# Kernel optimization log

Measured on AMD Instinct MI355X. Metric: run time of the kernel, lower is better.

Reference implementation:

```python
import jax, jax.numpy as jnp
import numpy as np
from jax import lax

EPS = 1e-06
NUM_FEATURES = 2048


def _welford(xr, mean0, var0):
    """Sequential Welford running mean/var, exactly matching the torch loop.

    xr: [N, F] rows processed one at a time.
    Update for the n-th observation (n starts at 1):
      if n > 1: var = (n-2)/(n-1)*var + (obs-mean)^2/n
      mean += (obs-mean)/n
    """
    n_rows = xr.shape[0]

    def step(carry, inp):
        mean, var = carry
        obs, n = inp
        nf = n.astype(xr.dtype)
        d = obs - mean
        # safe denominator so the unselected branch at n==1 is finite
        var_new = jnp.where(n > 1, (nf - 2.0) / jnp.maximum(nf - 1.0, 1.0) * var + d * d / nf, var)
        mean_new = mean + d / nf
        return (mean_new, var_new), None

    ns = jnp.arange(1, n_rows + 1, dtype=jnp.int32)
    (mean, var), _ = lax.scan(step, (mean0, var0), (xr, ns))
    return mean, var


def setup_inputs() -> dict:
    key = jax.random.key(0)
    x = jax.random.normal(key, (8192, NUM_FEATURES), dtype=jnp.float32)
    running_mean = jnp.zeros((NUM_FEATURES,), dtype=jnp.float32)
    running_var = jnp.ones((NUM_FEATURES,), dtype=jnp.float32)
    return {"x": x, "running_mean": running_mean, "running_var": running_var}


def reference(x, running_mean, running_var):
    xr = x.reshape(-1, NUM_FEATURES)
    mean, var = _welford(xr, running_mean, running_var)
    # normalize with the FINAL running stats (loop completes before return)
    return (x - mean) / jnp.sqrt(var + EPS)
```

## Files before the change

kernel.cpp:

```cpp
#include <hip/hip_runtime.h>

constexpr int F = 2048;
constexpr int NROWS = 8192;
constexpr float EPS = 1e-6f;
constexpr int STRIDE4 = F / 4;

__global__ __launch_bounds__(256) void reduce_kernel(const float* __restrict__ x,
                                                     float* __restrict__ acc) {
    __shared__ float4 lS[3 * 64];
    __shared__ float4 lQ[3 * 64];

    const int lc = threadIdx.x & 63;
    const int sg = threadIdx.x >> 6;
    const int c4 = blockIdx.x * 64 + lc;
    const int row0 = blockIdx.y * 64 + sg * 16;
    const float4* __restrict__ xv = reinterpret_cast<const float4*>(x);

    float4 s = make_float4(0.f, 0.f, 0.f, 0.f);
    float4 q = make_float4(0.f, 0.f, 0.f, 0.f);

    size_t base = (size_t)row0 * STRIDE4 + (size_t)c4;
#pragma unroll
    for (int r = 0; r < 16; ++r) {
        float4 v = xv[base + (size_t)r * STRIDE4];
        s.x += v.x;  s.y += v.y;  s.z += v.z;  s.w += v.w;
        q.x += v.x * v.x;  q.y += v.y * v.y;  q.z += v.z * v.z;  q.w += v.w * v.w;
    }

    if (sg != 0) {
        lS[(sg - 1) * 64 + lc] = s;
        lQ[(sg - 1) * 64 + lc] = q;
    }
    __syncthreads();

    if (sg == 0) {
#pragma unroll
        for (int k = 0; k < 3; ++k) {
            float4 t = lS[k * 64 + lc];
            float4 u = lQ[k * 64 + lc];
            s.x += t.x;  s.y += t.y;  s.z += t.z;  s.w += t.w;
            q.x += u.x;  q.y += u.y;  q.z += u.z;  q.w += u.w;
        }
        float* __restrict__ sum   = acc;
        float* __restrict__ sumsq = acc + F;
        const int c = c4 * 4;
        atomicAdd(&sum[c + 0], s.x);
        atomicAdd(&sum[c + 1], s.y);
        atomicAdd(&sum[c + 2], s.z);
        atomicAdd(&sum[c + 3], s.w);
        atomicAdd(&sumsq[c + 0], q.x);
        atomicAdd(&sumsq[c + 1], q.y);
        atomicAdd(&sumsq[c + 2], q.z);
        atomicAdd(&sumsq[c + 3], q.w);
    }
}

__global__ void finalize_kernel(const float* __restrict__ acc, float* __restrict__ stats) {
    const int c = blockIdx.x * blockDim.x + threadIdx.x;
    if (c < F) {
        const float s1 = acc[c];
        const float s2 = acc[c + F];
        const float invN = 1.0f / (float)NROWS;
        const float mean = s1 * invN;
        float var = (s2 - s1 * mean) * (1.0f / (float)(NROWS - 1));
        var = fmaxf(var, 0.0f);
        const float r = rsqrtf(var + EPS);
        stats[c]     = r;
        stats[c + F] = -mean * r;
    }
}

constexpr int TOTAL4 = NROWS * STRIDE4;
constexpr int HALF4  = TOTAL4 / 2;

__global__ __launch_bounds__(256) void normalize_kernel(const float* __restrict__ x,
                                                        const float* __restrict__ stats,
                                                        float* __restrict__ out) {
    const size_t i = (size_t)blockIdx.x * blockDim.x + threadIdx.x;
    const float4* __restrict__ xv = reinterpret_cast<const float4*>(x);
    float4* __restrict__ ov       = reinterpret_cast<float4*>(out);
    const float4* __restrict__ rv = reinterpret_cast<const float4*>(stats);
    const float4* __restrict__ bv = reinterpret_cast<const float4*>(stats + F);

#pragma unroll
    for (int h = 0; h < 2; ++h) {
        const size_t idx = i + (size_t)h * HALF4;
        const int c4 = (int)(idx & (STRIDE4 - 1));
        float4 v = xv[idx];
        float4 r = rv[c4];
        float4 b = bv[c4];
        float4 o;
        o.x = fmaf(v.x, r.x, b.x);
        o.y = fmaf(v.y, r.y, b.y);
        o.z = fmaf(v.z, r.z, b.z);
        o.w = fmaf(v.w, r.w, b.w);
        ov[idx] = o;
    }
}

extern "C" void kernel_launch(void* const* d_in, const int* in_sizes, int n_in,
                              void* d_out, int out_size, void* d_ws, size_t ws_size,
                              hipStream_t stream) {
    const float* x = (const float*)d_in[0];
    float* out   = (float*)d_out;
    float* acc   = (float*)d_ws;
    float* stats = acc + 2 * F;

    hipMemsetAsync(d_ws, 0, 2 * F * sizeof(float), stream);

    reduce_kernel<<<dim3(8, NROWS / 64), 256, 0, stream>>>(x, acc);
    finalize_kernel<<<F / 256, 256, 0, stream>>>(acc, stats);
    normalize_kernel<<<HALF4 / 256, 256, 0, stream>>>(x, stats, out);
}
```

Baseline: 131.2 us.

## Fuse finalize into normalize kernel and use nontemporal output stores

Removes the separate finalize kernel: each normalize thread now derives scale and bias for its four columns directly from the accumulated sums, and processes 16 rows with the same tiling as the reduce kernel. The output is written with nontemporal stores so it does not pollute cache, and the sum-of-squares accumulation uses fmaf. This saves one kernel launch and a round trip through the stats buffer, at the cost of redundant per-thread stat computation and a different access pattern in the normalize pass.

```diff
diff --git a/kernel.cpp b/kernel.cpp
--- a/kernel.cpp
+++ b/kernel.cpp
@@ -4,6 +4,8 @@
 constexpr int NROWS = 8192;
 constexpr float EPS = 1e-6f;
 constexpr int STRIDE4 = F / 4;
+
+typedef float nfloat4 __attribute__((ext_vector_type(4)));
 
 __global__ __launch_bounds__(256) void reduce_kernel(const float* __restrict__ x,
                                                      float* __restrict__ acc) {
@@ -24,7 +26,10 @@
     for (int r = 0; r < 16; ++r) {
         float4 v = xv[base + (size_t)r * STRIDE4];
         s.x += v.x;  s.y += v.y;  s.z += v.z;  s.w += v.w;
-        q.x += v.x * v.x;  q.y += v.y * v.y;  q.z += v.z * v.z;  q.w += v.w * v.w;
+        q.x = fmaf(v.x, v.x, q.x);
+        q.y = fmaf(v.y, v.y, q.y);
+        q.z = fmaf(v.z, v.z, q.z);
+        q.w = fmaf(v.w, v.w, q.w);
     }
 
     if (sg != 0) {
@@ -55,46 +60,53 @@
     }
 }
 
-__global__ void finalize_kernel(const float* __restrict__ acc, float* __restrict__ stats) {
-    const int c = blockIdx.x * blockDim.x + threadIdx.x;
-    if (c < F) {
-        const float s1 = acc[c];
-        const float s2 = acc[c + F];
-        const float invN = 1.0f / (float)NROWS;
-        const float mean = s1 * invN;
-        float var = (s2 - s1 * mean) * (1.0f / (float)(NROWS - 1));
-        var = fmaxf(var, 0.0f);
-        const float r = rsqrtf(var + EPS);
-        stats[c]     = r;
-        stats[c + F] = -mean * r;
+__global__ __launch_bounds__(256) void norm_kernel(const float* __restrict__ x,
+                                                   const float* __restrict__ acc,
+                                                   float* __restrict__ out) {
+    const int lc = threadIdx.x & 63;
+    const int sg = threadIdx.x >> 6;
+    const int c4 = blockIdx.x * 64 + lc;
+    const int row0 = blockIdx.y * 64 + sg * 16;
+    const float4* __restrict__ xv = reinterpret_cast<const float4*>(x);
+    nfloat4* __restrict__ ov      = reinterpret_cast<nfloat4*>(out);
+
+    const float4 S1 = reinterpret_cast<const float4*>(acc)[c4];
+    const float4 S2 = reinterpret_cast<const float4*>(acc + F)[c4];
+
+    const float invN  = 1.0f / (float)NROWS;
+    const float invN1 = 1.0f / (float)(NROWS - 1);
+
+    float4 r4, b4;
+    {
+        const float mx = S1.x * invN;
+        const float my = S1.y * invN;
+        const float mz = S1.z * invN;
+        const float mw = S1.w * invN;
+        const float vx = fmaxf((S2.x - S1.x * mx) * invN1, 0.0f);
+        const float vy = fmaxf((S2.y - S1.y * my) * invN1, 0.0f);
+        const float vz = fmaxf((S2.z - S1.z * mz) * invN1, 0.0f);
+        const float vw = fmaxf((S2.w - S1.w * mw) * invN1, 0.0f);
+        r4.x = rsqrtf(vx + EPS);
+        r4.y = rsqrtf(vy + EPS);
+        r4.z = rsqrtf(vz + EPS);
+        r4.w = rsqrtf(vw + EPS);
+        b4.x = -mx * r4.x;
+        b4.y = -my * r4.y;
+        b4.z = -mz * r4.z;
+        b4.w = -mw * r4.w;
     }
-}
 
-constexpr int TOTAL4 = NROWS * STRIDE4;
-constexpr int HALF4  = TOTAL4 / 2;
-
-__global__ __launch_bounds__(256) void normalize_kernel(const float* __restrict__ x,
-                                                        const float* __restrict__ stats,
-                                                        float* __restrict__ out) {
-    const size_t i = (size_t)blockIdx.x * blockDim.x + threadIdx.x;
-    const float4* __restrict__ xv = reinterpret_cast<const float4*>(x);
-    float4* __restrict__ ov       = reinterpret_cast<float4*>(out);
-    const float4* __restrict__ rv = reinterpret_cast<const float4*>(stats);
-    const float4* __restrict__ bv = reinterpret_cast<const float4*>(stats + F);
-
+    const size_t base = (size_t)row0 * STRIDE4 + (size_t)c4;
 #pragma unroll
-    for (int h = 0; h < 2; ++h) {
-        const size_t idx = i + (size_t)h * HALF4;
-        const int c4 = (int)(idx & (STRIDE4 - 1));
-        float4 v = xv[idx];
-        float4 r = rv[c4];
-        float4 b = bv[c4];
-        float4 o;
-        o.x = fmaf(v.x, r.x, b.x);
-        o.y = fmaf(v.y, r.y, b.y);
-        o.z = fmaf(v.z, r.z, b.z);
-        o.w = fmaf(v.w, r.w, b.w);
-        ov[idx] = o;
+    for (int r = 0; r < 16; ++r) {
+        const size_t idx = base + (size_t)r * STRIDE4;
+        const float4 t = xv[idx];
+        nfloat4 o;
+        o.x = fmaf(t.x, r4.x, b4.x);
+        o.y = fmaf(t.y, r4.y, b4.y);
+        o.z = fmaf(t.z, r4.z, b4.z);
+        o.w = fmaf(t.w, r4.w, b4.w);
+        __builtin_nontemporal_store(o, &ov[idx]);
     }
 }
 
@@ -102,13 +114,11 @@
                               void* d_out, int out_size, void* d_ws, size_t ws_size,
                               hipStream_t stream) {
     const float* x = (const float*)d_in[0];
-    float* out   = (float*)d_out;
-    float* acc   = (float*)d_ws;
-    float* stats = acc + 2 * F;
+    float* out = (float*)d_out;
+    float* acc = (float*)d_ws;
 
-    hipMemsetAsync(d_ws, 0, 2 * F * sizeof(float), stream);
+    (void)hipMemsetAsync(d_ws, 0, 2 * F * sizeof(float), stream);
 
     reduce_kernel<<<dim3(8, NROWS / 64), 256, 0, stream>>>(x, acc);
-    finalize_kernel<<<F / 256, 256, 0, stream>>>(acc, stats);
-    normalize_kernel<<<HALF4 / 256, 256, 0, stream>>>(x, stats, out);
+    norm_kernel<<<dim3(8, NROWS / 64), 256, 0, stream>>>(x, acc, out);
 }
```

Result: no change. 130.6 us (median of 2 runs) (-0.5%).
